# Kernel tuning notes

Hardware: AMD Instinct MI355X
Metric: run time of the kernel (lower is better)

The kernel has to match this reference:

```python
import jax, jax.numpy as jnp
import numpy as np

HARD_NUM = 700      # hardcoded self.hard_num in HardOIMLoss
OIM_SCALAR = 30.0   # oim_scalar init arg
N, D, P, Q = 4096, 256, 5532, 5000


def _l2norm(x):
    return x / jnp.linalg.norm(x, axis=-1, keepdims=True)


def setup_inputs() -> dict:
    key = jax.random.key(0)
    k1, k2, k3, k4, k5 = jax.random.split(key, 5)
    # OIM features and lookup tables are L2-normalized rows
    inputs = _l2norm(jax.random.normal(k1, (N, D), dtype=jnp.float32))
    lut = _l2norm(jax.random.normal(k2, (P, D), dtype=jnp.float32))
    cq = _l2norm(jax.random.normal(k3, (Q, D), dtype=jnp.float32))
    reliability = jax.random.uniform(k4, (P + Q,), dtype=jnp.float32)
    labels = jax.random.randint(k5, (N,), 0, P, dtype=jnp.int32)
    return {"inputs": inputs, "labels": labels, "lut": lut, "cq": cq,
            "reliability": reliability}


def reference(inputs, labels, lut, cq, reliability):
    # projected[n, c] = <inputs_n, table_c> * reliability_c ;  table = [lut; cq]
    table = jnp.concatenate([lut, cq], axis=0)            # [P+Q, D]
    projected = (inputs @ table.T) * reliability[None, :]  # [N, P+Q]
    C = projected.shape[1]
    # value at sorted-descending index HARD_NUM == (HARD_NUM+1)-th largest
    boundary = jax.lax.top_k(projected, HARD_NUM + 1)[0][:, -1]  # [N]
    hard_mask = projected >= boundary[:, None]
    label_mask = jnp.arange(C, dtype=labels.dtype)[None, :] == labels[:, None]
    mask = hard_mask | label_mask
    logits = jnp.where(mask, projected * OIM_SCALAR, -jnp.inf)
    # cross entropy (mean over rows); label column is always unmasked
    logZ = jax.scipy.special.logsumexp(logits, axis=1)
    tgt = jnp.take_along_axis(logits, labels[:, None].astype(jnp.int32), axis=1)[:, 0]
    return jnp.mean(logZ - tgt)
```

## Files before the change

### kernel.cpp

```cpp
#include <hip/hip_runtime.h>
#include <math.h>

#define N_ROWS 4096
#define DIM    256
#define P_SZ   5532
#define Q_SZ   5000
#define C_COLS 10532
#define TPAD   10624
#define PSTR   10624
#define NGR    (PSTR / 16)
#define K_SEL  701
#define SCALAR 30.0f
#define C2     (SCALAR * 1.4426950408889634f)

typedef __attribute__((ext_vector_type(8))) short   short8;
typedef __attribute__((ext_vector_type(4))) float   float4_t;
typedef __attribute__((ext_vector_type(4))) unsigned short ushort4_t;
typedef __attribute__((ext_vector_type(8))) unsigned short ushort8_t;
typedef __attribute__((ext_vector_type(4))) unsigned int  uint4_t;

__device__ __forceinline__ unsigned short f2bf(float f) {
    unsigned u = __float_as_uint(f);
    unsigned r = u + 0x7FFFu + ((u >> 16) & 1u);
    return (unsigned short)(r >> 16);
}
__device__ __forceinline__ float bf2f(unsigned short u) {
    return __uint_as_float((unsigned)u << 16);
}
__device__ __forceinline__ unsigned short key16(unsigned short u) {
    return (u & 0x8000u) ? (unsigned short)(~u) : (unsigned short)(u | 0x8000u);
}
__device__ __forceinline__ float key2f16(unsigned key) {
    unsigned short b = (key & 0x8000u) ? (unsigned short)(key & 0x7FFFu)
                                       : (unsigned short)(~key & 0xFFFFu);
    return bf2f(b);
}
__device__ __forceinline__ void gload16(const void* g, void* l) {
    __builtin_amdgcn_global_load_lds(
        (const __attribute__((address_space(1))) unsigned int*)g,
        (__attribute__((address_space(3))) unsigned int*)l, 16, 0, 0);
}

#define NIN_G  (N_ROWS * DIM / 4)
#define NTAB_G (TPAD * DIM / 4)

__global__ __launch_bounds__(256) void convert_bf16(
    const float* __restrict__ inputs, const float* __restrict__ lut,
    const float* __restrict__ cq, unsigned short* __restrict__ in_bf,
    unsigned short* __restrict__ tab_bf)
{
    const int g = blockIdx.x * 256 + threadIdx.x;
    if (g >= NIN_G + NTAB_G) return;
    float4_t v;
    unsigned short* dst;
    if (g < NIN_G) {
        v = *(const float4_t*)&inputs[(size_t)g * 4];
        dst = in_bf + (size_t)g * 4;
    } else {
        const int t = g - NIN_G;
        const int row = t >> 6;
        const int c4  = (t & 63) * 4;
        if (row < P_SZ)        v = *(const float4_t*)&lut[(size_t)row * DIM + c4];
        else if (row < C_COLS) v = *(const float4_t*)&cq[(size_t)(row - P_SZ) * DIM + c4];
        else                   v = (float4_t){0.f, 0.f, 0.f, 0.f};
        dst = tab_bf + (size_t)t * 4;
    }
    ushort4_t h = { f2bf(v.x), f2bf(v.y), f2bf(v.z), f2bf(v.w) };
    *(ushort4_t*)dst = h;
}

#define NWG_X 83
#define NWG_Y 32
#define NWG   (NWG_X * NWG_Y)
#define CSTR  132

__global__ __launch_bounds__(256) void gemm_proj(
    const unsigned short* __restrict__ in_bf,
    const unsigned short* __restrict__ tab_bf,
    const float* __restrict__ rel,
    unsigned short* __restrict__ proj)
{
    __shared__ __align__(16) unsigned short smem[128 * CSTR];

    const int tid  = threadIdx.x;
    const int lane = tid & 63, wid = tid >> 6;
    const int wm = wid >> 1, wn = wid & 1;

    const int phys = blockIdx.x;
    const int wg   = (phys & 7) * (NWG / 8) + (phys >> 3);
    const int bx   = wg >> 5;
    const int by   = wg & 31;
    const int row0 = by * 128, col0 = bx * 128;

    float4_t acc[4][4];
    #pragma unroll
    for (int i = 0; i < 4; ++i)
        #pragma unroll
        for (int j = 0; j < 4; ++j)
            acc[i][j] = (float4_t){0.f, 0.f, 0.f, 0.f};

    auto STAGE = [&](int b, int k0) {
        #pragma unroll
        for (int it = 0; it < 2; ++it) {
            const int g  = it * 256 + tid;
            const int r  = g >> 2;
            const int kb = ((g & 3) * 16) ^ ((r & 3) << 4);
            gload16(in_bf  + (size_t)(row0 + r) * DIM + k0 + (kb >> 1),
                    (char*)smem + b * 8192 + g * 16);
            gload16(tab_bf + (size_t)(col0 + r) * DIM + k0 + (kb >> 1),
                    (char*)smem + 16384 + b * 8192 + g * 16);
        }
    };

    STAGE(0, 0);
    #pragma unroll
    for (int t = 0; t < 8; ++t) {
        if (t < 7) {
            STAGE((t + 1) & 1, (t + 1) * 32);
            asm volatile("s_waitcnt vmcnt(4)" ::: "memory");
        } else {
            asm volatile("s_waitcnt vmcnt(0)" ::: "memory");
        }
        __builtin_amdgcn_s_barrier();

        const char* At = (const char*)smem + (t & 1) * 8192;
        const char* Bt = (const char*)smem + 16384 + (t & 1) * 8192;
        const int krow = lane & 15;
        const int kb   = (lane >> 4) << 4;
        short8 af[4], bfr[4];
        #pragma unroll
        for (int i = 0; i < 4; ++i) {
            const int r = wm * 64 + i * 16 + krow;
            af[i] = *(const short8*)(At + r * 64 + (kb ^ ((r & 3) << 4)));
        }
        #pragma unroll
        for (int j = 0; j < 4; ++j) {
            const int r = wn * 64 + j * 16 + krow;
            bfr[j] = *(const short8*)(Bt + r * 64 + (kb ^ ((r & 3) << 4)));
        }
        #pragma unroll
        for (int i = 0; i < 4; ++i)
            #pragma unroll
            for (int j = 0; j < 4; ++j)
                acc[i][j] = __builtin_amdgcn_mfma_f32_16x16x32_bf16(af[i], bfr[j], acc[i][j], 0, 0, 0);
        __builtin_amdgcn_s_barrier();
    }

    const int lr = (lane >> 4) << 2;
    const int lc = lane & 15;
    #pragma unroll
    for (int j = 0; j < 4; ++j) {
        const int cl  = wn * 64 + j * 16 + lc;
        const int col = col0 + cl;
        const bool pad = (col >= C_COLS);
        const float rl = pad ? 0.f : rel[col];
        #pragma unroll
        for (int i = 0; i < 4; ++i) {
            const int rbase = wm * 64 + i * 16 + lr;
            #pragma unroll
            for (int rr = 0; rr < 4; ++rr)
                smem[(rbase + rr) * CSTR + cl] =
                    pad ? (unsigned short)0u : key16(f2bf(acc[i][j][rr] * rl));
        }
    }
    __syncthreads();
    #pragma unroll
    for (int it = 0; it < 8; ++it) {
        const int g = it * 256 + tid;
        const int r = g >> 4;
        const int c8 = (g & 15) * 8;
        *(ushort8_t*)(proj + (size_t)(row0 + r) * PSTR + col0 + c8) =
            *(const ushort8_t*)&smem[r * CSTR + c8];
    }
}

#define SCAP  32
__global__ __launch_bounds__(256) void row_loss_kernel(
    const unsigned short* __restrict__ proj, const int* __restrict__ labels,
    float* __restrict__ row_loss)
{
    __shared__ unsigned short stash[SCAP * 256];
    __shared__ unsigned h2[256];
    __shared__ unsigned wsum[2][4];
    __shared__ float    fsum[4];
    __shared__ unsigned sel_sub, ovf;

    const int tid = threadIdx.x, lane = tid & 63, wid = tid >> 6;
    const int row = blockIdx.x;
    const uint4_t* prow = (const uint4_t*)(proj + (size_t)row * PSTR);

    h2[tid] = 0;
    if (tid == 0) ovf = 0;

    const bool tailv = (1280 + tid < NGR);
    uint4_t r0 = prow[tid];
    uint4_t r1 = prow[256 + tid];
    uint4_t r2 = prow[512 + tid];
    uint4_t r3 = prow[768 + tid];
    uint4_t r4 = prow[1024 + tid];
    uint4_t r5 = prow[tailv ? 1280 + tid : 1279];

    unsigned lo = 0, hi = 256, cnt_hi = 0;
    for (int pass = 0; pass < 8; ++pass) {
        const unsigned mid = (lo + hi) >> 1;
        const unsigned hiT = mid << 24;
        unsigned c = 0;
        auto CB = [&](unsigned w) {
            c += (unsigned)__popcll(__ballot(w >= hiT));
            c += (unsigned)__popcll(__ballot((w << 16) >= hiT));
        };
        #pragma unroll
        for (int d = 0; d < 4; ++d) CB(r0[d]);
        #pragma unroll
        for (int d = 0; d < 4; ++d) CB(r1[d]);
        #pragma unroll
        for (int d = 0; d < 4; ++d) CB(r2[d]);
        #pragma unroll
        for (int d = 0; d < 4; ++d) CB(r3[d]);
        #pragma unroll
        for (int d = 0; d < 4; ++d) CB(r4[d]);
        #pragma unroll
        for (int d = 0; d < 4; ++d) {
            c += (unsigned)__popcll(__ballot(tailv && (r5[d] >= hiT)));
            c += (unsigned)__popcll(__ballot(tailv && ((r5[d] << 16) >= hiT)));
        }
        if (lane == 0) wsum[pass & 1][wid] = c;
        __syncthreads();
        const unsigned total = wsum[pass & 1][0] + wsum[pass & 1][1]
                             + wsum[pass & 1][2] + wsum[pass & 1][3];
        if (total >= K_SEL) lo = mid;
        else { hi = mid; cnt_hi = total; }
    }
    const unsigned b1 = lo;
    const unsigned k2 = K_SEL - cnt_hi;
    const unsigned kfloor = b1 << 8;
    const unsigned kceil  = kfloor + 256u;

    unsigned cnt = 0;
    auto ST = [&](unsigned key) {
        if (key >= kfloor) {
            if (cnt < SCAP) stash[cnt * 256 + tid] = (unsigned short)key;
            else ovf = 1u;
            ++cnt;
        }
    };
    auto SW = [&](uint4_t w) {
        #pragma unroll
        for (int d = 0; d < 4; ++d) { ST(w[d] & 0xFFFFu); ST(w[d] >> 16); }
    };
    SW(r0); SW(r1); SW(r2); SW(r3); SW(r4);
    if (tailv) SW(r5);
    __syncthreads();

    float s = 0.f;
    unsigned bkey;
    if (ovf == 0) {
        for (unsigned c = 0; c < cnt; ++c) {
            const unsigned key = stash[c * 256 + tid];
            if (key < kceil) atomicAdd(&h2[key & 0xFFu], 1u);
        }
        __syncthreads();
        {
            const unsigned c = h2[tid];
            unsigned incl = c;
            #pragma unroll
            for (int off = 1; off < 64; off <<= 1) {
                const unsigned t = __shfl_down(incl, off, 64);
                if (lane + off < 64) incl += t;
            }
            if (lane == 0) wsum[0][wid] = incl;
            __syncthreads();
            unsigned above = incl - c;
            for (int w = wid + 1; w < 4; ++w) above += wsum[0][w];
            if (above < k2 && above + c >= k2) sel_sub = (unsigned)tid;
        }
        __syncthreads();
        bkey = kfloor | sel_sub;
        for (unsigned c = 0; c < cnt; ++c) {
            const unsigned key = stash[c * 256 + tid];
            if (key >= bkey) s += exp2f(C2 * key2f16(key) - C2);
        }
    } else {
        auto SB = [&](unsigned w) {
            const unsigned lv = w & 0xFFFFu, hv = w >> 16;
            if ((lv >> 8) == b1) atomicAdd(&h2[lv & 0xFFu], 1u);
            if ((hv >> 8) == b1) atomicAdd(&h2[hv & 0xFFu], 1u);
        };
        #pragma unroll
        for (int d = 0; d < 4; ++d) SB(r0[d]);
        #pragma unroll
        for (int d = 0; d < 4; ++d) SB(r1[d]);
        #pragma unroll
        for (int d = 0; d < 4; ++d) SB(r2[d]);
        #pragma unroll
        for (int d = 0; d < 4; ++d) SB(r3[d]);
        #pragma unroll
        for (int d = 0; d < 4; ++d) SB(r4[d]);
        if (tailv) {
            #pragma unroll
            for (int d = 0; d < 4; ++d) SB(r5[d]);
        }
        __syncthreads();
        {
            const unsigned c = h2[tid];
            unsigned incl = c;
            #pragma unroll
            for (int off = 1; off < 64; off <<= 1) {
                const unsigned t = __shfl_down(incl, off, 64);
                if (lane + off < 64) incl += t;
            }
            if (lane == 0) wsum[0][wid] = incl;
            __syncthreads();
            unsigned above = incl - c;
            for (int w = wid + 1; w < 4; ++w) above += wsum[0][w];
            if (above < k2 && above + c >= k2) sel_sub = (unsigned)tid;
        }
        __syncthreads();
        bkey = kfloor | sel_sub;
        auto EX = [&](unsigned w) {
            const unsigned lv = w & 0xFFFFu, hv = w >> 16;
            if (lv >= bkey) s += exp2f(C2 * key2f16(lv) - C2);
            if (hv >= bkey) s += exp2f(C2 * key2f16(hv) - C2);
        };
        #pragma unroll
        for (int d = 0; d < 4; ++d) EX(r0[d]);
        #pragma unroll
        for (int d = 0; d < 4; ++d) EX(r1[d]);
        #pragma unroll
        for (int d = 0; d < 4; ++d) EX(r2[d]);
        #pragma unroll
        for (int d = 0; d < 4; ++d) EX(r3[d]);
        #pragma unroll
        for (int d = 0; d < 4; ++d) EX(r4[d]);
        if (tailv) {
            #pragma unroll
            for (int d = 0; d < 4; ++d) EX(r5[d]);
        }
    }

    #pragma unroll
    for (int off = 1; off < 64; off <<= 1) {
        const float t = __shfl_down(s, off, 64);
        if (lane + off < 64) s += t;
    }
    if (lane == 0) fsum[wid] = s;
    __syncthreads();

    if (tid == 0) {
        float total = fsum[0] + fsum[1] + fsum[2] + fsum[3];
        const unsigned ulk = ((const unsigned short*)prow)[labels[row]];
        const float pl = key2f16(ulk);
        if (ulk < bkey) total += exp2f(C2 * pl - C2);
        row_loss[row] = SCALAR * 1.0f + logf(total) - SCALAR * pl;
    }
}

__global__ __launch_bounds__(256) void final_reduce(
    const float* __restrict__ row_loss, float* __restrict__ out)
{
    __shared__ float fred[4];
    const int tid = threadIdx.x, lane = tid & 63, wid = tid >> 6;
    float s = 0.f;
    for (int i = tid; i < N_ROWS; i += 256) s += row_loss[i];
    #pragma unroll
    for (int off = 1; off < 64; off <<= 1) {
        const float t = __shfl_down(s, off, 64);
        if (lane + off < 64) s += t;
    }
    if (lane == 0) fred[wid] = s;
    __syncthreads();
    if (tid == 0) out[0] = (fred[0] + fred[1] + fred[2] + fred[3]) / (float)N_ROWS;
}

extern "C" void kernel_launch(void* const* d_in, const int* in_sizes, int n_in,
                              void* d_out, int out_size, void* d_ws, size_t ws_size,
                              hipStream_t stream) {
    const float* inputs = (const float*)d_in[0];
    const int*   labels = (const int*)d_in[1];
    const float* lut    = (const float*)d_in[2];
    const float* cq     = (const float*)d_in[3];
    const float* rel    = (const float*)d_in[4];
    float* out = (float*)d_out;

    unsigned short* in_bf  = (unsigned short*)d_ws;
    unsigned short* tab_bf = in_bf  + (size_t)N_ROWS * DIM;
    unsigned short* proj   = tab_bf + (size_t)TPAD * DIM;
    float* rl_buf = (float*)(proj + (size_t)N_ROWS * PSTR);

    convert_bf16<<<(NIN_G + NTAB_G) / 256, 256, 0, stream>>>(inputs, lut, cq, in_bf, tab_bf);
    gemm_proj<<<NWG, 256, 0, stream>>>(in_bf, tab_bf, rel, proj);
    row_loss_kernel<<<N_ROWS, 256, 0, stream>>>(proj, labels, rl_buf);
    final_reduce<<<1, 256, 0, stream>>>(rl_buf, out);
}
```

Measured before the change: 96.30 us.

## Single-buffer GEMM LDS, process two rows per block, fuse final reduction via atomics

The GEMM drops its double-buffered K staging and splits the epilogue into two 64-row halves, roughly halving shared memory to allow more resident workgroups, at the cost of losing load/compute overlap. The row-loss kernel now handles two rows per block with both rows' data loaded up front. The separate final reduction kernel is replaced by per-row atomicAdd into a memset-zeroed output, which removes a launch but adds a memset and makes the summation order nondeterministic.

```diff
diff --git a/kernel.cpp b/kernel.cpp
--- a/kernel.cpp
+++ b/kernel.cpp
@@ -80,7 +80,7 @@
     const float* __restrict__ rel,
     unsigned short* __restrict__ proj)
 {
-    __shared__ __align__(16) unsigned short smem[128 * CSTR];
+    __shared__ __align__(16) unsigned short smem[64 * CSTR];
 
     const int tid  = threadIdx.x;
     const int lane = tid & 63, wid = tid >> 6;
@@ -99,32 +99,23 @@
         for (int j = 0; j < 4; ++j)
             acc[i][j] = (float4_t){0.f, 0.f, 0.f, 0.f};
 
-    auto STAGE = [&](int b, int k0) {
+    for (int t = 0; t < 8; ++t) {
+        const int k0 = t * 32;
         #pragma unroll
         for (int it = 0; it < 2; ++it) {
             const int g  = it * 256 + tid;
             const int r  = g >> 2;
             const int kb = ((g & 3) * 16) ^ ((r & 3) << 4);
             gload16(in_bf  + (size_t)(row0 + r) * DIM + k0 + (kb >> 1),
-                    (char*)smem + b * 8192 + g * 16);
+                    (char*)smem + g * 16);
             gload16(tab_bf + (size_t)(col0 + r) * DIM + k0 + (kb >> 1),
-                    (char*)smem + 16384 + b * 8192 + g * 16);
-        }
-    };
-
-    STAGE(0, 0);
-    #pragma unroll
-    for (int t = 0; t < 8; ++t) {
-        if (t < 7) {
-            STAGE((t + 1) & 1, (t + 1) * 32);
-            asm volatile("s_waitcnt vmcnt(4)" ::: "memory");
-        } else {
-            asm volatile("s_waitcnt vmcnt(0)" ::: "memory");
-        }
+                    (char*)smem + 8192 + g * 16);
+        }
+        asm volatile("s_waitcnt vmcnt(0)" ::: "memory");
         __builtin_amdgcn_s_barrier();
 
-        const char* At = (const char*)smem + (t & 1) * 8192;
-        const char* Bt = (const char*)smem + 16384 + (t & 1) * 8192;
+        const char* At = (const char*)smem;
+        const char* Bt = (const char*)smem + 8192;
         const int krow = lane & 15;
         const int kb   = (lane >> 4) << 4;
         short8 af[4], bfr[4];
@@ -149,35 +140,41 @@
     const int lr = (lane >> 4) << 2;
     const int lc = lane & 15;
     #pragma unroll
-    for (int j = 0; j < 4; ++j) {
-        const int cl  = wn * 64 + j * 16 + lc;
-        const int col = col0 + cl;
-        const bool pad = (col >= C_COLS);
-        const float rl = pad ? 0.f : rel[col];
-        #pragma unroll
-        for (int i = 0; i < 4; ++i) {
-            const int rbase = wm * 64 + i * 16 + lr;
-            #pragma unroll
-            for (int rr = 0; rr < 4; ++rr)
-                smem[(rbase + rr) * CSTR + cl] =
-                    pad ? (unsigned short)0u : key16(f2bf(acc[i][j][rr] * rl));
-        }
-    }
-    __syncthreads();
-    #pragma unroll
-    for (int it = 0; it < 8; ++it) {
-        const int g = it * 256 + tid;
-        const int r = g >> 4;
-        const int c8 = (g & 15) * 8;
-        *(ushort8_t*)(proj + (size_t)(row0 + r) * PSTR + col0 + c8) =
-            *(const ushort8_t*)&smem[r * CSTR + c8];
+    for (int h = 0; h < 2; ++h) {
+        if (wm == h) {
+            #pragma unroll
+            for (int j = 0; j < 4; ++j) {
+                const int cl  = wn * 64 + j * 16 + lc;
+                const int col = col0 + cl;
+                const bool pad = (col >= C_COLS);
+                const float rl = pad ? 0.f : rel[col];
+                #pragma unroll
+                for (int i = 0; i < 4; ++i) {
+                    const int rbase = i * 16 + lr;
+                    #pragma unroll
+                    for (int rr = 0; rr < 4; ++rr)
+                        smem[(rbase + rr) * CSTR + cl] =
+                            pad ? (unsigned short)0u : key16(f2bf(acc[i][j][rr] * rl));
+                }
+            }
+        }
+        __syncthreads();
+        #pragma unroll
+        for (int it = 0; it < 4; ++it) {
+            const int g = it * 256 + tid;
+            const int r = g >> 4;
+            const int c8 = (g & 15) * 8;
+            *(ushort8_t*)(proj + (size_t)(row0 + h * 64 + r) * PSTR + col0 + c8) =
+                *(const ushort8_t*)&smem[r * CSTR + c8];
+        }
+        __syncthreads();
     }
 }
 
 #define SCAP  32
 __global__ __launch_bounds__(256) void row_loss_kernel(
     const unsigned short* __restrict__ proj, const int* __restrict__ labels,
-    float* __restrict__ row_loss)
+    float* __restrict__ out)
 {
     __shared__ unsigned short stash[SCAP * 256];
     __shared__ unsigned h2[256];
@@ -186,190 +183,179 @@
     __shared__ unsigned sel_sub, ovf;
 
     const int tid = threadIdx.x, lane = tid & 63, wid = tid >> 6;
-    const int row = blockIdx.x;
-    const uint4_t* prow = (const uint4_t*)(proj + (size_t)row * PSTR);
-
-    h2[tid] = 0;
-    if (tid == 0) ovf = 0;
-
+    const int rowA = blockIdx.x * 2, rowB = rowA + 1;
     const bool tailv = (1280 + tid < NGR);
-    uint4_t r0 = prow[tid];
-    uint4_t r1 = prow[256 + tid];
-    uint4_t r2 = prow[512 + tid];
-    uint4_t r3 = prow[768 + tid];
-    uint4_t r4 = prow[1024 + tid];
-    uint4_t r5 = prow[tailv ? 1280 + tid : 1279];
-
-    unsigned lo = 0, hi = 256, cnt_hi = 0;
-    for (int pass = 0; pass < 8; ++pass) {
-        const unsigned mid = (lo + hi) >> 1;
-        const unsigned hiT = mid << 24;
-        unsigned c = 0;
-        auto CB = [&](unsigned w) {
-            c += (unsigned)__popcll(__ballot(w >= hiT));
-            c += (unsigned)__popcll(__ballot((w << 16) >= hiT));
+    const uint4_t* pA = (const uint4_t*)(proj + (size_t)rowA * PSTR);
+    const uint4_t* pB = (const uint4_t*)(proj + (size_t)rowB * PSTR);
+
+    uint4_t a0 = pA[tid],        a1 = pA[256 + tid],  a2 = pA[512 + tid];
+    uint4_t a3 = pA[768 + tid],  a4 = pA[1024 + tid], a5 = pA[tailv ? 1280 + tid : 1279];
+    uint4_t b0 = pB[tid],        b1 = pB[256 + tid],  b2 = pB[512 + tid];
+    uint4_t b3 = pB[768 + tid],  b4 = pB[1024 + tid], b5 = pB[tailv ? 1280 + tid : 1279];
+
+    auto PROC = [&](uint4_t r0, uint4_t r1, uint4_t r2, uint4_t r3, uint4_t r4,
+                    uint4_t r5, const uint4_t* prow, int row) {
+        h2[tid] = 0;
+        if (tid == 0) ovf = 0;
+
+        unsigned lo = 0, hi = 256, cnt_hi = 0;
+        for (int pass = 0; pass < 8; ++pass) {
+            const unsigned mid = (lo + hi) >> 1;
+            const unsigned hiT = mid << 24;
+            unsigned c = 0;
+            auto CB = [&](unsigned w) {
+                c += (unsigned)__popcll(__ballot(w >= hiT));
+                c += (unsigned)__popcll(__ballot((w << 16) >= hiT));
+            };
+            #pragma unroll
+            for (int d = 0; d < 4; ++d) CB(r0[d]);
+            #pragma unroll
+            for (int d = 0; d < 4; ++d) CB(r1[d]);
+            #pragma unroll
+            for (int d = 0; d < 4; ++d) CB(r2[d]);
+            #pragma unroll
+            for (int d = 0; d < 4; ++d) CB(r3[d]);
+            #pragma unroll
+            for (int d = 0; d < 4; ++d) CB(r4[d]);
+            #pragma unroll
+            for (int d = 0; d < 4; ++d) {
+                c += (unsigned)__popcll(__ballot(tailv && (r5[d] >= hiT)));
+                c += (unsigned)__popcll(__ballot(tailv && ((r5[d] << 16) >= hiT)));
+            }
+            if (lane == 0) wsum[pass & 1][wid] = c;
+            __syncthreads();
+            const unsigned total = wsum[pass & 1][0] + wsum[pass & 1][1]
+                                 + wsum[pass & 1][2] + wsum[pass & 1][3];
+            if (total >= K_SEL) lo = mid;
+            else { hi = mid; cnt_hi = total; }
+        }
+        const unsigned b1b = lo;
+        const unsigned k2 = K_SEL - cnt_hi;
+        const unsigned kfloor = b1b << 8;
+        const unsigned kceil  = kfloor + 256u;
+
+        unsigned cnt = 0;
+        auto ST = [&](unsigned key) {
+            if (key >= kfloor) {
+                if (cnt < SCAP) stash[cnt * 256 + tid] = (unsigned short)key;
+                else ovf = 1u;
+                ++cnt;
+            }
         };
-        #pragma unroll
-        for (int d = 0; d < 4; ++d) CB(r0[d]);
-        #pragma unroll
-        for (int d = 0; d < 4; ++d) CB(r1[d]);
-        #pragma unroll
-        for (int d = 0; d < 4; ++d) CB(r2[d]);
-        #pragma unroll
-        for (int d = 0; d < 4; ++d) CB(r3[d]);
-        #pragma unroll
-        for (int d = 0; d < 4; ++d) CB(r4[d]);
-        #pragma unroll
-        for (int d = 0; d < 4; ++d) {
-            c += (unsigned)__popcll(__ballot(tailv && (r5[d] >= hiT)));
-            c += (unsigned)__popcll(__ballot(tailv && ((r5[d] << 16) >= hiT)));
-        }
-        if (lane == 0) wsum[pass & 1][wid] = c;
-        __syncthreads();
-        const unsigned total = wsum[pass & 1][0] + wsum[pass & 1][1]
-                             + wsum[pass & 1][2] + wsum[pass & 1][3];
-        if (total >= K_SEL) lo = mid;
-        else { hi = mid; cnt_hi = total; }
-    }
-    const unsigned b1 = lo;
-    const unsigned k2 = K_SEL - cnt_hi;
-    const unsigned kfloor = b1 << 8;
-    const unsigned kceil  = kfloor + 256u;
-
-    unsigned cnt = 0;
-    auto ST = [&](unsigned key) {
-        if (key >= kfloor) {
-            if (cnt < SCAP) stash[cnt * 256 + tid] = (unsigned short)key;
-            else ovf = 1u;
-            ++cnt;
-        }
+        auto SW = [&](uint4_t w) {
+            #pragma unroll
+            for (int d = 0; d < 4; ++d) { ST(w[d] & 0xFFFFu); ST(w[d] >> 16); }
+        };
+        SW(r0); SW(r1); SW(r2); SW(r3); SW(r4);
+        if (tailv) SW(r5);
+        __syncthreads();
+
+        float s = 0.f;
+        unsigned bkey;
+        if (ovf == 0) {
+            for (unsigned c = 0; c < cnt; ++c) {
+                const unsigned key = stash[c * 256 + tid];
+                if (key < kceil) atomicAdd(&h2[key & 0xFFu], 1u);
+            }
+            __syncthreads();
+            {
+                const unsigned c = h2[tid];
+                unsigned incl = c;
+                #pragma unroll
+                for (int off = 1; off < 64; off <<= 1) {
+                    const unsigned t = __shfl_down(incl, off, 64);
+                    if (lane + off < 64) incl += t;
+                }
+                if (lane == 0) wsum[0][wid] = incl;
+                __syncthreads();
+                unsigned above = incl - c;
+                for (int w = wid + 1; w < 4; ++w) above += wsum[0][w];
+                if (above < k2 && above + c >= k2) sel_sub = (unsigned)tid;
+            }
+            __syncthreads();
+            bkey = kfloor | sel_sub;
+            for (unsigned c = 0; c < cnt; ++c) {
+                const unsigned key = stash[c * 256 + tid];
+                if (key >= bkey) s += exp2f(C2 * key2f16(key) - C2);
+            }
+        } else {
+            auto SB = [&](unsigned w) {
+                const unsigned lv = w & 0xFFFFu, hv = w >> 16;
+                if ((lv >> 8) == b1b) atomicAdd(&h2[lv & 0xFFu], 1u);
+                if ((hv >> 8) == b1b) atomicAdd(&h2[hv & 0xFFu], 1u);
+            };
+            #pragma unroll
+            for (int d = 0; d < 4; ++d) SB(r0[d]);
+            #pragma unroll
+            for (int d = 0; d < 4; ++d) SB(r1[d]);
+            #pragma unroll
+            for (int d = 0; d < 4; ++d) SB(r2[d]);
+            #pragma unroll
+            for (int d = 0; d < 4; ++d) SB(r3[d]);
+            #pragma unroll
+            for (int d = 0; d < 4; ++d) SB(r4[d]);
+            if (tailv) {
+                #pragma unroll
+                for (int d = 0; d < 4; ++d) SB(r5[d]);
+            }
+            __syncthreads();
+            {
+                const unsigned c = h2[tid];
+                unsigned incl = c;
+                #pragma unroll
+                for (int off = 1; off < 64; off <<= 1) {
+                    const unsigned t = __shfl_down(incl, off, 64);
+                    if (lane + off < 64) incl += t;
+                }
+                if (lane == 0) wsum[0][wid] = incl;
+                __syncthreads();
+                unsigned above = incl - c;
+                for (int w = wid + 1; w < 4; ++w) above += wsum[0][w];
+                if (above < k2 && above + c >= k2) sel_sub = (unsigned)tid;
+            }
+            __syncthreads();
+            bkey = kfloor | sel_sub;
+            auto EX = [&](unsigned w) {
+                const unsigned lv = w & 0xFFFFu, hv = w >> 16;
+                if (lv >= bkey) s += exp2f(C2 * key2f16(lv) - C2);
+                if (hv >= bkey) s += exp2f(C2 * key2f16(hv) - C2);
+            };
+            #pragma unroll
+            for (int d = 0; d < 4; ++d) EX(r0[d]);
+            #pragma unroll
+            for (int d = 0; d < 4; ++d) EX(r1[d]);
+            #pragma unroll
+            for (int d = 0; d < 4; ++d) EX(r2[d]);
+            #pragma unroll
+            for (int d = 0; d < 4; ++d) EX(r3[d]);
+            #pragma unroll
+            for (int d = 0; d < 4; ++d) EX(r4[d]);
+            if (tailv) {
+                #pragma unroll
+                for (int d = 0; d < 4; ++d) EX(r5[d]);
+            }
+        }
+
+        #pragma unroll
+        for (int off = 1; off < 64; off <<= 1) {
+            const float t = __shfl_down(s, off, 64);
+            if (lane + off < 64) s += t;
+        }
+        if (lane == 0) fsum[wid] = s;
+        __syncthreads();
+        if (tid == 0) {
+            float total = fsum[0] + fsum[1] + fsum[2] + fsum[3];
+            const unsigned ulk = ((const unsigned short*)prow)[labels[row]];
+            const float pl = key2f16(ulk);
+            if (ulk < bkey) total += exp2f(C2 * pl - C2);
+            const float loss = SCALAR * 1.0f + logf(total) - SCALAR * pl;
+            atomicAdd(out, loss * (1.0f / (float)N_ROWS));
+        }
+        __syncthreads();
     };
-    auto SW = [&](uint4_t w) {
-        #pragma unroll
-        for (int d = 0; d < 4; ++d) { ST(w[d] & 0xFFFFu); ST(w[d] >> 16); }
-    };
-    SW(r0); SW(r1); SW(r2); SW(r3); SW(r4);
-    if (tailv) SW(r5);
-    __syncthreads();
-
-    float s = 0.f;
-    unsigned bkey;
-    if (ovf == 0) {
-        for (unsigned c = 0; c < cnt; ++c) {
-            const unsigned key = stash[c * 256 + tid];
-            if (key < kceil) atomicAdd(&h2[key & 0xFFu], 1u);
-        }
-        __syncthreads();
-        {
-            const unsigned c = h2[tid];
-            unsigned incl = c;
-            #pragma unroll
-            for (int off = 1; off < 64; off <<= 1) {
-                const unsigned t = __shfl_down(incl, off, 64);
-                if (lane + off < 64) incl += t;
-            }
-            if (lane == 0) wsum[0][wid] = incl;
-            __syncthreads();
-            unsigned above = incl - c;
-            for (int w = wid + 1; w < 4; ++w) above += wsum[0][w];
-            if (above < k2 && above + c >= k2) sel_sub = (unsigned)tid;
-        }
-        __syncthreads();
-        bkey = kfloor | sel_sub;
-        for (unsigned c = 0; c < cnt; ++c) {
-            const unsigned key = stash[c * 256 + tid];
-            if (key >= bkey) s += exp2f(C2 * key2f16(key) - C2);
-        }
-    } else {
-        auto SB = [&](unsigned w) {
-            const unsigned lv = w & 0xFFFFu, hv = w >> 16;
-            if ((lv >> 8) == b1) atomicAdd(&h2[lv & 0xFFu], 1u);
-            if ((hv >> 8) == b1) atomicAdd(&h2[hv & 0xFFu], 1u);
-        };
-        #pragma unroll
-        for (int d = 0; d < 4; ++d) SB(r0[d]);
-        #pragma unroll
-        for (int d = 0; d < 4; ++d) SB(r1[d]);
-        #pragma unroll
-        for (int d = 0; d < 4; ++d) SB(r2[d]);
-        #pragma unroll
-        for (int d = 0; d < 4; ++d) SB(r3[d]);
-        #pragma unroll
-        for (int d = 0; d < 4; ++d) SB(r4[d]);
-        if (tailv) {
-            #pragma unroll
-            for (int d = 0; d < 4; ++d) SB(r5[d]);
-        }
-        __syncthreads();
-        {
-            const unsigned c = h2[tid];
-            unsigned incl = c;
-            #pragma unroll
-            for (int off = 1; off < 64; off <<= 1) {
-                const unsigned t = __shfl_down(incl, off, 64);
-                if (lane + off < 64) incl += t;
-            }
-            if (lane == 0) wsum[0][wid] = incl;
-            __syncthreads();
-            unsigned above = incl - c;
-            for (int w = wid + 1; w < 4; ++w) above += wsum[0][w];
-            if (above < k2 && above + c >= k2) sel_sub = (unsigned)tid;
-        }
-        __syncthreads();
-        bkey = kfloor | sel_sub;
-        auto EX = [&](unsigned w) {
-            const unsigned lv = w & 0xFFFFu, hv = w >> 16;
-            if (lv >= bkey) s += exp2f(C2 * key2f16(lv) - C2);
-            if (hv >= bkey) s += exp2f(C2 * key2f16(hv) - C2);
-        };
-        #pragma unroll
-        for (int d = 0; d < 4; ++d) EX(r0[d]);
-        #pragma unroll
-        for (int d = 0; d < 4; ++d) EX(r1[d]);
-        #pragma unroll
-        for (int d = 0; d < 4; ++d) EX(r2[d]);
-        #pragma unroll
-        for (int d = 0; d < 4; ++d) EX(r3[d]);
-        #pragma unroll
-        for (int d = 0; d < 4; ++d) EX(r4[d]);
-        if (tailv) {
-            #pragma unroll
-            for (int d = 0; d < 4; ++d) EX(r5[d]);
-        }
-    }
-
-    #pragma unroll
-    for (int off = 1; off < 64; off <<= 1) {
-        const float t = __shfl_down(s, off, 64);
-        if (lane + off < 64) s += t;
-    }
-    if (lane == 0) fsum[wid] = s;
-    __syncthreads();
-
-    if (tid == 0) {
-        float total = fsum[0] + fsum[1] + fsum[2] + fsum[3];
-        const unsigned ulk = ((const unsigned short*)prow)[labels[row]];
-        const float pl = key2f16(ulk);
-        if (ulk < bkey) total += exp2f(C2 * pl - C2);
-        row_loss[row] = SCALAR * 1.0f + logf(total) - SCALAR * pl;
-    }
-}
-
-__global__ __launch_bounds__(256) void final_reduce(
-    const float* __restrict__ row_loss, float* __restrict__ out)
-{
-    __shared__ float fred[4];
-    const int tid = threadIdx.x, lane = tid & 63, wid = tid >> 6;
-    float s = 0.f;
-    for (int i = tid; i < N_ROWS; i += 256) s += row_loss[i];
-    #pragma unroll
-    for (int off = 1; off < 64; off <<= 1) {
-        const float t = __shfl_down(s, off, 64);
-        if (lane + off < 64) s += t;
-    }
-    if (lane == 0) fred[wid] = s;
-    __syncthreads();
-    if (tid == 0) out[0] = (fred[0] + fred[1] + fred[2] + fred[3]) / (float)N_ROWS;
+
+    PROC(a0, a1, a2, a3, a4, a5, pA, rowA);
+    PROC(b0, b1, b2, b3, b4, b5, pB, rowB);
 }
 
 extern "C" void kernel_launch(void* const* d_in, const int* in_sizes, int n_in,
@@ -385,10 +371,9 @@
     unsigned short* in_bf  = (unsigned short*)d_ws;
     unsigned short* tab_bf = in_bf  + (size_t)N_ROWS * DIM;
     unsigned short* proj   = tab_bf + (size_t)TPAD * DIM;
-    float* rl_buf = (float*)(proj + (size_t)N_ROWS * PSTR);
-
+
+    hipMemsetAsync(out, 0, sizeof(float), stream);
     convert_bf16<<<(NIN_G + NTAB_G) / 256, 256, 0, stream>>>(inputs, lut, cq, in_bf, tab_bf);
     gemm_proj<<<NWG, 256, 0, stream>>>(in_bf, tab_bf, rel, proj);
-    row_loss_kernel<<<N_ROWS, 256, 0, stream>>>(proj, labels, rl_buf);
-    final_reduce<<<1, 256, 0, stream>>>(rl_buf, out);
-}
+    row_loss_kernel<<<N_ROWS / 2, 256, 0, stream>>>(proj, labels, out);
+}
```

Result: slower. 146.3 us (+51.9%).
